# Kernel tuning notes

Measured on AMD Instinct MI355X. Metric: run time of the kernel, lower is better.

## Reference

```python
import jax, jax.numpy as jnp
import numpy as np

B, H, P, L = 8, 128, 128, 4096


def _cplx(x):
    # view_as_complex: (..., 2) float -> complex
    return x[..., 0] + 1j * x[..., 1]


def setup_inputs() -> dict:
    key = jax.random.key(0)
    ks = jax.random.split(key, 6)
    u = jax.random.normal(ks[0], (B, H, L), dtype=jnp.float32)
    C_ri = jax.random.normal(ks[1], (H, P, 2), dtype=jnp.float32)
    D_ri = jax.random.normal(ks[2], (H, H, 2), dtype=jnp.float32)
    # ContinuousStateReservoir: Re(Lambda) in [high_stability, low_stability] = [-1.0, -0.1]
    lam_re = jax.random.uniform(ks[3], (P,), minval=-1.0, maxval=-0.1, dtype=jnp.float32)
    lam_im = jax.random.normal(ks[4], (P,), dtype=jnp.float32) * np.float32(np.pi)
    Lam = lam_re + 1j * lam_im                      # continuous eigs
    Lam_bar = jnp.exp(Lam)                          # ZOH with Delta = 1
    B0 = jax.random.normal(ks[5], (P, H, 2), dtype=jnp.float32)
    Bc = _cplx(B0)
    B_bar = ((Lam_bar - 1.0) / Lam)[:, None] * Bc   # ZOH B_bar
    B_ri = jnp.stack([B_bar.real, B_bar.imag], axis=-1).astype(jnp.float32)
    Lambda_ri = jnp.stack([Lam_bar.real, Lam_bar.imag], axis=-1).astype(jnp.float32)
    return {"u": u, "C_ri": C_ri, "D_ri": D_ri, "B_ri": B_ri, "Lambda_ri": Lambda_ri}


def reference(u, C_ri, D_ri, B_ri, Lambda_ri):
    C = _cplx(C_ri)          # (H, P) complex
    D = _cplx(D_ri)          # (H, H)
    B_bar = _cplx(B_ri)      # (P, H)
    Lam_bar = _cplx(Lambda_ri)  # (P,)
    # torch.fft.rfftn defaults to ALL dims: complex FFT on (B,H), real FFT on L
    U_s = jnp.fft.rfftn(u)                                   # (B, H, Lf)
    s = 1j * (2.0 * jnp.pi * jnp.fft.rfftfreq(u.shape[-1]))  # (Lf,)
    mid = 1.0 / (s[None, :] - Lam_bar[:, None])              # (P, Lf) Cauchy kernel
    C_mid = jnp.einsum('hp,pl->hpl', C, mid)                 # (H, P, Lf)
    G = jnp.einsum('hpl,pq->hql', C_mid, B_bar)              # (H, H, Lf) transfer function
    Y_s = jnp.einsum('hql,bql->bhl', G, U_s) + jnp.einsum('hq,bql->bhl', D, U_s)
    y = jnp.fft.irfftn(Y_s)                                  # (B, H, L) real
    return jax.nn.gelu(y, approximate=False)
```

## Files before the change

### kernel.cpp

```cpp
#include <hip/hip_runtime.h>
#include <math.h>

#define Bn 8
#define Hn 128
#define Pn 128
#define Ln 4096
#define LF 2049
#define NROWS (Bn*Hn)
#define NT 32
#define NTILES 65
#define PLSZ 4096
#define WPLSZ 16384
#define TSCALE 64.0f

#define SKEW(a) ((a) + ((a) >> 4))
#define FBUF 2176

typedef _Float16 f16x8 __attribute__((ext_vector_type(8)));
typedef float f32x4 __attribute__((ext_vector_type(4)));

__device__ __forceinline__ void fsincos(float a, float* s, float* c) {
    *s = __sinf(a);
    *c = __cosf(a);
}

__device__ __forceinline__ void write2(_Float16* __restrict__ W, int idx,
                                       float vr, float vi) {
    W[0 * WPLSZ + idx] = (_Float16)vr;
    W[1 * WPLSZ + idx] = (_Float16)vi;
}

__global__ void prep_ABE_k(const float* __restrict__ B_ri, const float* __restrict__ C_ri,
                           const float* __restrict__ D_ri,
                           _Float16* __restrict__ W1, _Float16* __restrict__ W2,
                           float2* __restrict__ E) {
    int bid = blockIdx.x;
    int idx = (bid & 63) * 256 + threadIdx.x;
    int rrow = idx >> 7, ccol = idx & 127;
    if (bid < 64) {
        float sr = 0.f, si = 0.f;
        for (int q = 0; q < 128; ++q) {
            float br = B_ri[(rrow * 128 + q) * 2 + 0];
            float bi = B_ri[(rrow * 128 + q) * 2 + 1];
            float ang = -3.14159265358979f * (float)((q * ccol) & 127) / 64.0f;
            float sw, cw; fsincos(ang, &sw, &cw);
            sr += br * cw - bi * sw;
            si += br * sw + bi * cw;
        }
        write2(W1, idx, sr, si);
    } else if (bid < 128) {
        float sr = 0.f, si = 0.f;
        for (int h2 = 0; h2 < 128; ++h2) {
            float cr = C_ri[(h2 * 128 + ccol) * 2 + 0];
            float ci = C_ri[(h2 * 128 + ccol) * 2 + 1];
            float ang = 3.14159265358979f * (float)((rrow * h2) & 127) / 64.0f;
            float sw, cw; fsincos(ang, &sw, &cw);
            sr += cr * cw - ci * sw;
            si += cr * sw + ci * cw;
        }
        write2(W2, idx, sr * (TSCALE / 128.0f), si * (TSCALE / 128.0f));
    } else {
        float sr = 0.f, si = 0.f;
        for (int c = 0; c < 128; ++c) {
            float dr = D_ri[(rrow * 128 + c) * 2 + 0];
            float di = D_ri[(rrow * 128 + c) * 2 + 1];
            float ang = -3.14159265358979f * (float)((c * ccol) & 127) / 64.0f;
            float sw, cw; fsincos(ang, &sw, &cw);
            sr += dr * cw - di * sw;
            si += dr * sw + di * cw;
        }
        E[idx] = make_float2(sr, si);
    }
}

__global__ void prep_W3_k(const float2* __restrict__ E, _Float16* __restrict__ W3) {
    int idx = blockIdx.x * blockDim.x + threadIdx.x;
    int h = idx >> 7, q = idx & 127;
    float sr = 0.f, si = 0.f;
    for (int a = 0; a < 128; ++a) {
        float2 e = E[a * 128 + q];
        float ang = 3.14159265358979f * (float)((h * a) & 127) / 64.0f;
        float sw, cw; fsincos(ang, &sw, &cw);
        sr += e.x * cw - e.y * sw;
        si += e.x * sw + e.y * cw;
    }
    write2(W3, idx, sr * (1.0f / 128.0f), si * (1.0f / 128.0f));
}

__device__ __forceinline__ float2 cadd2(float2 a, float2 b) { return make_float2(a.x + b.x, a.y + b.y); }
__device__ __forceinline__ float2 csub2(float2 a, float2 b) { return make_float2(a.x - b.x, a.y - b.y); }

template <int SIGN>
__device__ __forceinline__ void dft4(float2 a0, float2 a1, float2 a2, float2 a3,
                                     float2& y0, float2& y1, float2& y2, float2& y3) {
    float t0x = a0.x + a2.x, t0y = a0.y + a2.y;
    float t1x = a0.x - a2.x, t1y = a0.y - a2.y;
    float t2x = a1.x + a3.x, t2y = a1.y + a3.y;
    float t3x = a1.x - a3.x, t3y = a1.y - a3.y;
    y0 = make_float2(t0x + t2x, t0y + t2y);
    y2 = make_float2(t0x - t2x, t0y - t2y);
    y1 = make_float2(t1x - (float)SIGN * t3y, t1y + (float)SIGN * t3x);
    y3 = make_float2(t1x + (float)SIGN * t3y, t1y - (float)SIGN * t3x);
}

template <int SIGN>
__device__ __forceinline__ void fft2048(float2* bufA, float2* bufB) {
    const int tid = threadIdx.x;
    float2* src = bufA;
    float2* dst = bufB;
    #pragma unroll
    for (int stg = 0; stg < 3; ++stg) {
        const int ls = 3 * stg;
        const int k = tid;
        const int q = k & ((1 << ls) - 1);
        const int p = k >> ls;
        float2 a[8];
        #pragma unroll
        for (int u = 0; u < 8; ++u) a[u] = src[SKEW(k + (u << 8))];
        float2 A0, A1, A2, A3, B0, B1, B2, B3;
        dft4<SIGN>(a[0], a[2], a[4], a[6], A0, A1, A2, A3);
        dft4<SIGN>(a[1], a[3], a[5], a[7], B0, B1, B2, B3);
        const float c45 = 0.70710678118655f;
        float2 w1 = make_float2(c45 * (B1.x - (float)SIGN * B1.y), c45 * ((float)SIGN * B1.x + B1.y));
        float2 w2 = make_float2(-(float)SIGN * B2.y, (float)SIGN * B2.x);
        float2 w3 = make_float2(c45 * (-B3.x - (float)SIGN * B3.y), c45 * ((float)SIGN * B3.x - B3.y));
        float2 b[8];
        b[0] = cadd2(A0, B0);  b[4] = csub2(A0, B0);
        b[1] = cadd2(A1, w1);  b[5] = csub2(A1, w1);
        b[2] = cadd2(A2, w2);  b[6] = csub2(A2, w2);
        b[3] = cadd2(A3, w3);  b[7] = csub2(A3, w3);
        float ang = (float)SIGN * 6.28318530717959f * (float)p * (1.0f / (float)(2048 >> ls));
        #pragma unroll
        for (int j = 1; j < 8; ++j) {
            float sj, cj; fsincos((float)j * ang, &sj, &cj);
            b[j] = make_float2(b[j].x * cj - b[j].y * sj, b[j].x * sj + b[j].y * cj);
        }
        const int base = q + (p << (ls + 3));
        #pragma unroll
        for (int j = 0; j < 8; ++j) dst[SKEW(base + (j << ls))] = b[j];
        __syncthreads();
        float2* t = src; src = dst; dst = t;
    }
    #pragma unroll
    for (int r = 0; r < 2; ++r) {
        int k = tid + (r << 8);
        float2 a0 = src[SKEW(k)];
        float2 a1 = src[SKEW(k + 512)];
        float2 a2 = src[SKEW(k + 1024)];
        float2 a3 = src[SKEW(k + 1536)];
        float2 y0, y1, y2, y3;
        dft4<SIGN>(a0, a1, a2, a3, y0, y1, y2, y3);
        dst[SKEW(k)] = y0;
        dst[SKEW(k + 512)] = y1;
        dst[SKEW(k + 1024)] = y2;
        dst[SKEW(k + 1536)] = y3;
    }
    __syncthreads();
}

__global__ __launch_bounds__(256, 4) void rfft_rows_k(const float* __restrict__ u,
                                                      float2* __restrict__ Uhat) {
    __shared__ __align__(16) float2 bufA[FBUF];
    __shared__ __align__(16) float2 bufB[FBUF];
    const int row = blockIdx.x;
    const int tid = threadIdx.x;
    const float4* up4 = (const float4*)(u + (size_t)row * Ln);
    #pragma unroll
    for (int r = 0; r < 4; ++r) {
        float4 v = up4[tid + (r << 8)];
        int i = 2 * (tid + (r << 8));
        bufA[SKEW(i)] = make_float2(v.x, v.y);
        bufA[SKEW(i + 1)] = make_float2(v.z, v.w);
    }
    __syncthreads();
    fft2048<-1>(bufA, bufB);
    float2* op = Uhat + (size_t)row * LF;
    for (int l = tid; l < 1025; l += 256) {
        float2 Zl = bufA[SKEW(l)];
        float2 Zm = bufA[SKEW((2048 - l) & 2047)];
        float2 Fe = make_float2(0.5f * (Zl.x + Zm.x), 0.5f * (Zl.y - Zm.y));
        float2 Dv = make_float2(0.5f * (Zl.x - Zm.x), 0.5f * (Zl.y + Zm.y));
        float2 Fo = make_float2(Dv.y, -Dv.x);
        float s, c; fsincos(-3.14159265358979f * (float)l / 2048.0f, &s, &c);
        float2 TF = make_float2(Fo.x * c - Fo.y * s, Fo.x * s + Fo.y * c);
        op[l] = make_float2(Fe.x + TF.x, Fe.y + TF.y);
        op[2048 - l] = make_float2(Fe.x - TF.x, -(Fe.y - TF.y));
    }
}

__global__ __launch_bounds__(256, 4) void irfft_gelu_k(const float2* __restrict__ Uhat,
                                                       float* __restrict__ out) {
    __shared__ __align__(16) float2 bufA[FBUF];
    __shared__ __align__(16) float2 bufB[FBUF];
    const int row = blockIdx.x;
    const int tid = threadIdx.x;
    const float2* wp = Uhat + (size_t)row * LF;
    for (int l = tid; l < 1025; l += 256) {
        float2 Ul = wp[l];
        float2 Um = wp[2048 - l];
        float2 Fe = make_float2(0.5f * (Ul.x + Um.x), 0.5f * (Ul.y - Um.y));
        float2 Dv = make_float2(0.5f * (Ul.x - Um.x), 0.5f * (Ul.y + Um.y));
        float s, c; fsincos(3.14159265358979f * (float)l / 2048.0f, &s, &c);
        float2 Fo = make_float2(Dv.x * c - Dv.y * s, Dv.x * s + Dv.y * c);
        bufA[SKEW(l)] = make_float2(Fe.x - Fo.y, Fe.y + Fo.x);
        if (l >= 1 && l <= 1023)
            bufA[SKEW(2048 - l)] = make_float2(Fe.x + Fo.y, Fo.x - Fe.y);
    }
    __syncthreads();
    fft2048<1>(bufA, bufB);
    float4* op4 = (float4*)(out + (size_t)row * Ln);
    #pragma unroll
    for (int r = 0; r < 4; ++r) {
        int n = 2 * (tid + (r << 8));
        float2 z0 = bufA[SKEW(n)];
        float2 z1 = bufA[SKEW(n + 1)];
        float y0 = z0.x * (1.0f / 2048.0f);
        float y1 = z0.y * (1.0f / 2048.0f);
        float y2 = z1.x * (1.0f / 2048.0f);
        float y3 = z1.y * (1.0f / 2048.0f);
        op4[tid + (r << 8)] = make_float4(
            0.5f * y0 * (1.0f + erff(y0 * 0.70710678118655f)),
            0.5f * y1 * (1.0f + erff(y1 * 0.70710678118655f)),
            0.5f * y2 * (1.0f + erff(y2 * 0.70710678118655f)),
            0.5f * y3 * (1.0f + erff(y3 * 0.70710678118655f)));
    }
}

__device__ __forceinline__ f32x4 mfma16h(f16x8 a, f16x8 b, f32x4 c) {
    return __builtin_amdgcn_mfma_f32_16x16x32_f16(a, b, c, 0, 0, 0);
}
__device__ __forceinline__ f16x8 read_frag(const _Float16* plane, int n, int k) {
    int ksw = k ^ ((n & 7) << 3);
    return *(const f16x8*)(plane + n * 128 + ksw);
}
__device__ __forceinline__ f16x8 aread(const _Float16* W, int pl, int m, int k) {
    return *(const f16x8*)(W + pl * WPLSZ + m * 128 + k);
}

__global__ __launch_bounds__(256, 4) void mixmm_k(float2* __restrict__ Uhat,
                                                  const _Float16* __restrict__ W1,
                                                  const _Float16* __restrict__ W2,
                                                  const _Float16* __restrict__ W3,
                                                  const float* __restrict__ Lam) {
    __shared__ __align__(16) _Float16 Up[2 * PLSZ];
    __shared__ __align__(16) _Float16 Tp[2 * PLSZ];

    const int tid = threadIdx.x;
    const int b = blockIdx.x / NTILES;
    const int tile = blockIdx.x % NTILES;
    const int l0 = tile * NT;
    const int ncols = (LF - l0) < NT ? (LF - l0) : NT;

    {
        int n = tid & 31, kc = tid >> 5;
        float2 v[16];
        #pragma unroll
        for (int j = 0; j < 16; ++j) {
            int h = kc * 16 + j;
            v[j] = (n < ncols) ? Uhat[(size_t)(b * 128 + h) * LF + l0 + n]
                               : make_float2(0.f, 0.f);
        }
        #pragma unroll
        for (int jc = 0; jc < 2; ++jc) {
            f16x8 fr, fi;
            #pragma unroll
            for (int j = 0; j < 8; ++j) {
                fr[j] = (_Float16)v[jc * 8 + j].x;
                fi[j] = (_Float16)v[jc * 8 + j].y;
            }
            int ksw = (kc * 16 + jc * 8) ^ ((n & 7) << 3);
            *(f16x8*)(Up + 0 * PLSZ + n * 128 + ksw) = fr;
            *(f16x8*)(Up + 1 * PLSZ + n * 128 + ksw) = fi;
        }
    }
    __syncthreads();

    const int lane = tid & 63;
    const int w = tid >> 6;
    const int m15 = lane & 15;
    const int quad = lane >> 4;

    f32x4 accR[2][2], accM[2][2], accI[2][2];
    #pragma unroll
    for (int s = 0; s < 2; ++s)
        #pragma unroll
        for (int t = 0; t < 2; ++t) {
            accR[s][t] = (f32x4)0.f; accM[s][t] = (f32x4)0.f; accI[s][t] = (f32x4)0.f;
        }

    #pragma unroll
    for (int kb = 0; kb < 4; ++kb) {
        int k = kb * 32 + quad * 8;
        f16x8 wr[2], wi[2];
        #pragma unroll
        for (int s = 0; s < 2; ++s) {
            int m = w * 32 + s * 16 + m15;
            wr[s] = aread(W1, 0, m, k);
            wi[s] = aread(W1, 1, m, k);
        }
        f16x8 br[2], bi[2];
        #pragma unroll
        for (int t = 0; t < 2; ++t) {
            br[t] = read_frag(Up + 0 * PLSZ, t * 16 + m15, k);
            bi[t] = read_frag(Up + 1 * PLSZ, t * 16 + m15, k);
        }
        #pragma unroll
        for (int s = 0; s < 2; ++s)
            #pragma unroll
            for (int t = 0; t < 2; ++t) {
                accR[s][t] = mfma16h(wr[s], br[t], accR[s][t]);
                accM[s][t] = mfma16h(wi[s], bi[t], accM[s][t]);
                accI[s][t] = mfma16h(wr[s], bi[t], accI[s][t]);
                accI[s][t] = mfma16h(wi[s], br[t], accI[s][t]);
            }
    }

    #pragma unroll
    for (int s = 0; s < 2; ++s) {
        #pragma unroll
        for (int reg = 0; reg < 4; ++reg) {
            int p = w * 32 + s * 16 + quad * 4 + reg;
            float2 lamv = ((const float2*)Lam)[p];
            float dr = -lamv.x;
            #pragma unroll
            for (int t = 0; t < 2; ++t) {
                int n = t * 16 + m15;
                int l = l0 + n;
                float di = 3.14159265358979f * (float)l / 2048.0f - lamv.y;
                float inv = (1.0f / TSCALE) / (dr * dr + di * di);
                float xr = accR[s][t][reg] - accM[s][t][reg];
                float xi = accI[s][t][reg];
                float tr = (xr * dr + xi * di) * inv;
                float ti = (xi * dr - xr * di) * inv;
                int off = n * 128 + (p ^ ((n & 7) << 3));
                Tp[0 * PLSZ + off] = (_Float16)tr;
                Tp[1 * PLSZ + off] = (_Float16)ti;
            }
        }
    }
    __syncthreads();

    #pragma unroll
    for (int s = 0; s < 2; ++s)
        #pragma unroll
        for (int t = 0; t < 2; ++t) {
            accR[s][t] = (f32x4)0.f; accM[s][t] = (f32x4)0.f; accI[s][t] = (f32x4)0.f;
        }

    #pragma unroll
    for (int kb = 0; kb < 4; ++kb) {
        int k = kb * 32 + quad * 8;
        {
            f16x8 wr[2], wi[2];
            #pragma unroll
            for (int s = 0; s < 2; ++s) {
                int m = w * 32 + s * 16 + m15;
                wr[s] = aread(W2, 0, m, k);
                wi[s] = aread(W2, 1, m, k);
            }
            f16x8 br[2], bi[2];
            #pragma unroll
            for (int t = 0; t < 2; ++t) {
                br[t] = read_frag(Tp + 0 * PLSZ, t * 16 + m15, k);
                bi[t] = read_frag(Tp + 1 * PLSZ, t * 16 + m15, k);
            }
            #pragma unroll
            for (int s = 0; s < 2; ++s)
                #pragma unroll
                for (int t = 0; t < 2; ++t) {
                    accR[s][t] = mfma16h(wr[s], br[t], accR[s][t]);
                    accM[s][t] = mfma16h(wi[s], bi[t], accM[s][t]);
                    accI[s][t] = mfma16h(wr[s], bi[t], accI[s][t]);
                    accI[s][t] = mfma16h(wi[s], br[t], accI[s][t]);
                }
        }
        {
            f16x8 wr[2], wi[2];
            #pragma unroll
            for (int s = 0; s < 2; ++s) {
                int m = w * 32 + s * 16 + m15;
                wr[s] = aread(W3, 0, m, k);
                wi[s] = aread(W3, 1, m, k);
            }
            f16x8 br[2], bi[2];
            #pragma unroll
            for (int t = 0; t < 2; ++t) {
                br[t] = read_frag(Up + 0 * PLSZ, t * 16 + m15, k);
                bi[t] = read_frag(Up + 1 * PLSZ, t * 16 + m15, k);
            }
            #pragma unroll
            for (int s = 0; s < 2; ++s)
                #pragma unroll
                for (int t = 0; t < 2; ++t) {
                    accR[s][t] = mfma16h(wr[s], br[t], accR[s][t]);
                    accM[s][t] = mfma16h(wi[s], bi[t], accM[s][t]);
                    accI[s][t] = mfma16h(wr[s], bi[t], accI[s][t]);
                    accI[s][t] = mfma16h(wi[s], br[t], accI[s][t]);
                }
        }
    }

    #pragma unroll
    for (int s = 0; s < 2; ++s) {
        #pragma unroll
        for (int t = 0; t < 2; ++t) {
            int n = t * 16 + m15;
            if (n < ncols) {
                #pragma unroll
                for (int reg = 0; reg < 4; ++reg) {
                    int m = w * 32 + s * 16 + quad * 4 + reg;
                    Uhat[(size_t)(b * 128 + m) * LF + l0 + n] =
                        make_float2(accR[s][t][reg] - accM[s][t][reg], accI[s][t][reg]);
                }
            }
        }
    }
}

extern "C" void kernel_launch(void* const* d_in, const int* in_sizes, int n_in,
                              void* d_out, int out_size, void* d_ws, size_t ws_size,
                              hipStream_t stream) {
    const float* u    = (const float*)d_in[0];
    const float* C_ri = (const float*)d_in[1];
    const float* D_ri = (const float*)d_in[2];
    const float* B_ri = (const float*)d_in[3];
    const float* Lam  = (const float*)d_in[4];
    float* out = (float*)d_out;

    float2* Uhat = (float2*)d_ws;
    _Float16* W1 = (_Float16*)(Uhat + (size_t)NROWS * LF);
    _Float16* W2 = W1 + 2 * WPLSZ;
    _Float16* W3 = W2 + 2 * WPLSZ;
    float2* Em = (float2*)(W3 + 2 * WPLSZ);

    prep_ABE_k<<<192, 256, 0, stream>>>(B_ri, C_ri, D_ri, W1, W2, Em);
    prep_W3_k<<<64, 256, 0, stream>>>(Em, W3);

    rfft_rows_k<<<NROWS, 256, 0, stream>>>(u, Uhat);
    mixmm_k<<<Bn * NTILES, 256, 0, stream>>>(Uhat, W1, W2, W3, Lam);
    irfft_gelu_k<<<NROWS, 256, 0, stream>>>(Uhat, out);
}
```

Baseline: 144.5 us.

## Make FFT in-place with single LDS buffer and replace sincos with twiddle recurrences

The 2048-point FFT now works in place on one shared buffer, with an extra barrier between the loads and stores of each stage. This halves LDS use per block, and launch bounds are raised to allow 6 blocks per CU. Per-element sin/cos calls in the FFT twiddles, the real-FFT post/pre-processing and the prep DFT kernels are replaced by complex multiplication recurrences. This cuts transcendental work but adds rounding drift and one more sync per stage.

After: 143.3 us. About the same (-0.9%).

```diff
diff --git a/kernel.cpp b/kernel.cpp
--- a/kernel.cpp
+++ b/kernel.cpp
@@ -24,10 +24,42 @@
     *c = __cosf(a);
 }
 
+__device__ __forceinline__ float2 cmulff(float2 a, float2 b) {
+    return make_float2(a.x * b.x - a.y * b.y, a.x * b.y + a.y * b.x);
+}
+
 __device__ __forceinline__ void write2(_Float16* __restrict__ W, int idx,
                                        float vr, float vi) {
     W[0 * WPLSZ + idx] = (_Float16)vr;
     W[1 * WPLSZ + idx] = (_Float16)vi;
+}
+
+__device__ __forceinline__ void dftsum(const float* __restrict__ src, int stride,
+                                       float ang, float& outr, float& outi) {
+    float stepi, stepr;
+    fsincos(ang, &stepi, &stepr);
+    float s2r = stepr * stepr - stepi * stepi;
+    float s2i = 2.0f * stepr * stepi;
+    float w0r = 1.0f, w0i = 0.0f;
+    float w1r = stepr, w1i = stepi;
+    float sr = 0.f, si = 0.f, tr = 0.f, ti = 0.f;
+    #pragma unroll 4
+    for (int q = 0; q < 128; q += 2) {
+        float ar = src[q * stride], ai = src[q * stride + 1];
+        sr += ar * w0r - ai * w0i;
+        si += ar * w0i + ai * w0r;
+        float n0 = w0r * s2r - w0i * s2i;
+        w0i = w0r * s2i + w0i * s2r;
+        w0r = n0;
+        float br = src[(q + 1) * stride], bi = src[(q + 1) * stride + 1];
+        tr += br * w1r - bi * w1i;
+        ti += br * w1i + bi * w1r;
+        float n1 = w1r * s2r - w1i * s2i;
+        w1i = w1r * s2i + w1i * s2r;
+        w1r = n1;
+    }
+    outr = sr + tr;
+    outi = si + ti;
 }
 
 __global__ void prep_ABE_k(const float* __restrict__ B_ri, const float* __restrict__ C_ri,
@@ -38,37 +70,16 @@
     int idx = (bid & 63) * 256 + threadIdx.x;
     int rrow = idx >> 7, ccol = idx & 127;
     if (bid < 64) {
-        float sr = 0.f, si = 0.f;
-        for (int q = 0; q < 128; ++q) {
-            float br = B_ri[(rrow * 128 + q) * 2 + 0];
-            float bi = B_ri[(rrow * 128 + q) * 2 + 1];
-            float ang = -3.14159265358979f * (float)((q * ccol) & 127) / 64.0f;
-            float sw, cw; fsincos(ang, &sw, &cw);
-            sr += br * cw - bi * sw;
-            si += br * sw + bi * cw;
-        }
+        float sr, si;
+        dftsum(B_ri + rrow * 256, 2, -3.14159265358979f * (float)ccol / 64.0f, sr, si);
         write2(W1, idx, sr, si);
     } else if (bid < 128) {
-        float sr = 0.f, si = 0.f;
-        for (int h2 = 0; h2 < 128; ++h2) {
-            float cr = C_ri[(h2 * 128 + ccol) * 2 + 0];
-            float ci = C_ri[(h2 * 128 + ccol) * 2 + 1];
-            float ang = 3.14159265358979f * (float)((rrow * h2) & 127) / 64.0f;
-            float sw, cw; fsincos(ang, &sw, &cw);
-            sr += cr * cw - ci * sw;
-            si += cr * sw + ci * cw;
-        }
+        float sr, si;
+        dftsum(C_ri + ccol * 2, 256, 3.14159265358979f * (float)rrow / 64.0f, sr, si);
         write2(W2, idx, sr * (TSCALE / 128.0f), si * (TSCALE / 128.0f));
     } else {
-        float sr = 0.f, si = 0.f;
-        for (int c = 0; c < 128; ++c) {
-            float dr = D_ri[(rrow * 128 + c) * 2 + 0];
-            float di = D_ri[(rrow * 128 + c) * 2 + 1];
-            float ang = -3.14159265358979f * (float)((c * ccol) & 127) / 64.0f;
-            float sw, cw; fsincos(ang, &sw, &cw);
-            sr += dr * cw - di * sw;
-            si += dr * sw + di * cw;
-        }
+        float sr, si;
+        dftsum(D_ri + rrow * 256, 2, -3.14159265358979f * (float)ccol / 64.0f, sr, si);
         E[idx] = make_float2(sr, si);
     }
 }
@@ -76,14 +87,8 @@
 __global__ void prep_W3_k(const float2* __restrict__ E, _Float16* __restrict__ W3) {
     int idx = blockIdx.x * blockDim.x + threadIdx.x;
     int h = idx >> 7, q = idx & 127;
-    float sr = 0.f, si = 0.f;
-    for (int a = 0; a < 128; ++a) {
-        float2 e = E[a * 128 + q];
-        float ang = 3.14159265358979f * (float)((h * a) & 127) / 64.0f;
-        float sw, cw; fsincos(ang, &sw, &cw);
-        sr += e.x * cw - e.y * sw;
-        si += e.x * sw + e.y * cw;
-    }
+    float sr, si;
+    dftsum((const float*)E + q * 2, 256, 3.14159265358979f * (float)h / 64.0f, sr, si);
     write2(W3, idx, sr * (1.0f / 128.0f), si * (1.0f / 128.0f));
 }
 
@@ -104,64 +109,70 @@
 }
 
 template <int SIGN>
-__device__ __forceinline__ void fft2048(float2* bufA, float2* bufB) {
+__device__ __forceinline__ void fft2048_ip(float2* buf) {
     const int tid = threadIdx.x;
-    float2* src = bufA;
-    float2* dst = bufB;
     #pragma unroll
     for (int stg = 0; stg < 3; ++stg) {
         const int ls = 3 * stg;
-        const int k = tid;
-        const int q = k & ((1 << ls) - 1);
-        const int p = k >> ls;
+        const int q = tid & ((1 << ls) - 1);
+        const int p = tid >> ls;
         float2 a[8];
         #pragma unroll
-        for (int u = 0; u < 8; ++u) a[u] = src[SKEW(k + (u << 8))];
+        for (int u = 0; u < 8; ++u) a[u] = buf[SKEW(tid + (u << 8))];
+        __syncthreads();
         float2 A0, A1, A2, A3, B0, B1, B2, B3;
         dft4<SIGN>(a[0], a[2], a[4], a[6], A0, A1, A2, A3);
         dft4<SIGN>(a[1], a[3], a[5], a[7], B0, B1, B2, B3);
         const float c45 = 0.70710678118655f;
-        float2 w1 = make_float2(c45 * (B1.x - (float)SIGN * B1.y), c45 * ((float)SIGN * B1.x + B1.y));
-        float2 w2 = make_float2(-(float)SIGN * B2.y, (float)SIGN * B2.x);
-        float2 w3 = make_float2(c45 * (-B3.x - (float)SIGN * B3.y), c45 * ((float)SIGN * B3.x - B3.y));
+        float2 w1v = make_float2(c45 * (B1.x - (float)SIGN * B1.y), c45 * ((float)SIGN * B1.x + B1.y));
+        float2 w2v = make_float2(-(float)SIGN * B2.y, (float)SIGN * B2.x);
+        float2 w3v = make_float2(c45 * (-B3.x - (float)SIGN * B3.y), c45 * ((float)SIGN * B3.x - B3.y));
         float2 b[8];
         b[0] = cadd2(A0, B0);  b[4] = csub2(A0, B0);
-        b[1] = cadd2(A1, w1);  b[5] = csub2(A1, w1);
-        b[2] = cadd2(A2, w2);  b[6] = csub2(A2, w2);
-        b[3] = cadd2(A3, w3);  b[7] = csub2(A3, w3);
+        b[1] = cadd2(A1, w1v); b[5] = csub2(A1, w1v);
+        b[2] = cadd2(A2, w2v); b[6] = csub2(A2, w2v);
+        b[3] = cadd2(A3, w3v); b[7] = csub2(A3, w3v);
         float ang = (float)SIGN * 6.28318530717959f * (float)p * (1.0f / (float)(2048 >> ls));
-        #pragma unroll
-        for (int j = 1; j < 8; ++j) {
-            float sj, cj; fsincos((float)j * ang, &sj, &cj);
-            b[j] = make_float2(b[j].x * cj - b[j].y * sj, b[j].x * sj + b[j].y * cj);
-        }
+        float st, ct; fsincos(ang, &st, &ct);
+        float2 T1 = make_float2(ct, st);
+        float2 T2 = cmulff(T1, T1);
+        float2 T3 = cmulff(T2, T1);
+        float2 T4 = cmulff(T2, T2);
+        float2 T5 = cmulff(T4, T1);
+        float2 T6 = cmulff(T4, T2);
+        float2 T7 = cmulff(T4, T3);
+        b[1] = cmulff(b[1], T1);
+        b[2] = cmulff(b[2], T2);
+        b[3] = cmulff(b[3], T3);
+        b[4] = cmulff(b[4], T4);
+        b[5] = cmulff(b[5], T5);
+        b[6] = cmulff(b[6], T6);
+        b[7] = cmulff(b[7], T7);
         const int base = q + (p << (ls + 3));
         #pragma unroll
-        for (int j = 0; j < 8; ++j) dst[SKEW(base + (j << ls))] = b[j];
+        for (int j = 0; j < 8; ++j) buf[SKEW(base + (j << ls))] = b[j];
         __syncthreads();
-        float2* t = src; src = dst; dst = t;
     }
     #pragma unroll
     for (int r = 0; r < 2; ++r) {
         int k = tid + (r << 8);
-        float2 a0 = src[SKEW(k)];
-        float2 a1 = src[SKEW(k + 512)];
-        float2 a2 = src[SKEW(k + 1024)];
-        float2 a3 = src[SKEW(k + 1536)];
+        float2 a0 = buf[SKEW(k)];
+        float2 a1 = buf[SKEW(k + 512)];
+        float2 a2 = buf[SKEW(k + 1024)];
+        float2 a3 = buf[SKEW(k + 1536)];
         float2 y0, y1, y2, y3;
         dft4<SIGN>(a0, a1, a2, a3, y0, y1, y2, y3);
-        dst[SKEW(k)] = y0;
-        dst[SKEW(k + 512)] = y1;
-        dst[SKEW(k + 1024)] = y2;
-        dst[SKEW(k + 1536)] = y3;
+        buf[SKEW(k)] = y0;
+        buf[SKEW(k + 512)] = y1;
+        buf[SKEW(k + 1024)] = y2;
+        buf[SKEW(k + 1536)] = y3;
     }
     __syncthreads();
 }
 
-__global__ __launch_bounds__(256, 4) void rfft_rows_k(const float* __restrict__ u,
+__global__ __launch_bounds__(256, 6) void rfft_rows_k(const float* __restrict__ u,
                                                       float2* __restrict__ Uhat) {
-    __shared__ __align__(16) float2 bufA[FBUF];
-    __shared__ __align__(16) float2 bufB[FBUF];
+    __shared__ __align__(16) float2 buf[FBUF];
     const int row = blockIdx.x;
     const int tid = threadIdx.x;
     const float4* up4 = (const float4*)(u + (size_t)row * Ln);
@@ -169,51 +180,60 @@
     for (int r = 0; r < 4; ++r) {
         float4 v = up4[tid + (r << 8)];
         int i = 2 * (tid + (r << 8));
-        bufA[SKEW(i)] = make_float2(v.x, v.y);
-        bufA[SKEW(i + 1)] = make_float2(v.z, v.w);
+        buf[SKEW(i)] = make_float2(v.x, v.y);
+        buf[SKEW(i + 1)] = make_float2(v.z, v.w);
     }
     __syncthreads();
-    fft2048<-1>(bufA, bufB);
+    fft2048_ip<-1>(buf);
     float2* op = Uhat + (size_t)row * LF;
+    float s, c;
+    fsincos(-3.14159265358979f * (float)tid / 2048.0f, &s, &c);
+    const float c8 = 0.92387953251129f, s8 = -0.38268343236509f;
     for (int l = tid; l < 1025; l += 256) {
-        float2 Zl = bufA[SKEW(l)];
-        float2 Zm = bufA[SKEW((2048 - l) & 2047)];
+        float2 Zl = buf[SKEW(l)];
+        float2 Zm = buf[SKEW((2048 - l) & 2047)];
         float2 Fe = make_float2(0.5f * (Zl.x + Zm.x), 0.5f * (Zl.y - Zm.y));
         float2 Dv = make_float2(0.5f * (Zl.x - Zm.x), 0.5f * (Zl.y + Zm.y));
         float2 Fo = make_float2(Dv.y, -Dv.x);
-        float s, c; fsincos(-3.14159265358979f * (float)l / 2048.0f, &s, &c);
         float2 TF = make_float2(Fo.x * c - Fo.y * s, Fo.x * s + Fo.y * c);
         op[l] = make_float2(Fe.x + TF.x, Fe.y + TF.y);
         op[2048 - l] = make_float2(Fe.x - TF.x, -(Fe.y - TF.y));
-    }
-}
-
-__global__ __launch_bounds__(256, 4) void irfft_gelu_k(const float2* __restrict__ Uhat,
+        float cn = c * c8 - s * s8;
+        s = c * s8 + s * c8;
+        c = cn;
+    }
+}
+
+__global__ __launch_bounds__(256, 6) void irfft_gelu_k(const float2* __restrict__ Uhat,
                                                        float* __restrict__ out) {
-    __shared__ __align__(16) float2 bufA[FBUF];
-    __shared__ __align__(16) float2 bufB[FBUF];
+    __shared__ __align__(16) float2 buf[FBUF];
     const int row = blockIdx.x;
     const int tid = threadIdx.x;
     const float2* wp = Uhat + (size_t)row * LF;
+    float s, c;
+    fsincos(3.14159265358979f * (float)tid / 2048.0f, &s, &c);
+    const float c8 = 0.92387953251129f, s8 = 0.38268343236509f;
     for (int l = tid; l < 1025; l += 256) {
         float2 Ul = wp[l];
         float2 Um = wp[2048 - l];
         float2 Fe = make_float2(0.5f * (Ul.x + Um.x), 0.5f * (Ul.y - Um.y));
         float2 Dv = make_float2(0.5f * (Ul.x - Um.x), 0.5f * (Ul.y + Um.y));
-        float s, c; fsincos(3.14159265358979f * (float)l / 2048.0f, &s, &c);
         float2 Fo = make_float2(Dv.x * c - Dv.y * s, Dv.x * s + Dv.y * c);
-        bufA[SKEW(l)] = make_float2(Fe.x - Fo.y, Fe.y + Fo.x);
+        buf[SKEW(l)] = make_float2(Fe.x - Fo.y, Fe.y + Fo.x);
         if (l >= 1 && l <= 1023)
-            bufA[SKEW(2048 - l)] = make_float2(Fe.x + Fo.y, Fo.x - Fe.y);
+            buf[SKEW(2048 - l)] = make_float2(Fe.x + Fo.y, Fo.x - Fe.y);
+        float cn = c * c8 - s * s8;
+        s = c * s8 + s * c8;
+        c = cn;
     }
     __syncthreads();
-    fft2048<1>(bufA, bufB);
+    fft2048_ip<1>(buf);
     float4* op4 = (float4*)(out + (size_t)row * Ln);
     #pragma unroll
     for (int r = 0; r < 4; ++r) {
         int n = 2 * (tid + (r << 8));
-        float2 z0 = bufA[SKEW(n)];
-        float2 z1 = bufA[SKEW(n + 1)];
+        float2 z0 = buf[SKEW(n)];
+        float2 z1 = buf[SKEW(n + 1)];
         float y0 = z0.x * (1.0f / 2048.0f);
         float y1 = z0.y * (1.0f / 2048.0f);
         float y2 = z1.x * (1.0f / 2048.0f);
```
